# Performance work log

Measured on AMD Instinct MI355X. Metric: run time of the kernel, lower is better.

Reference implementation:

```python
import jax, jax.numpy as jnp
import numpy as np

KH, KW, STRIDE, PAD = 3, 3, 1, 1


def unfold(img, kh, kw, stride, padding):
    # torch.nn.functional.unfold, transposed to [B, L, C*kh*kw] with (c, kh, kw)-major ordering
    b, c, h, w = img.shape
    p = jnp.pad(img, ((0, 0), (0, 0), (padding, padding), (padding, padding)))
    oh = (h - kh + 2 * padding) // stride + 1
    ow = (w - kw + 2 * padding) // stride + 1
    # [b, c, kh*kw, oh, ow]; static python loop over the 9 kernel offsets only
    cols = jnp.stack([p[:, :, i:i + oh * stride:stride, j:j + ow * stride:stride]
                      for i in range(kh) for j in range(kw)], axis=2)
    return cols.reshape(b, c * kh * kw, oh * ow).transpose(0, 2, 1), oh, ow


def setup_inputs() -> dict:
    key = jax.random.key(0)
    k1, k2 = jax.random.split(key)
    img = jax.random.normal(k1, (8, 64, 112, 112), dtype=jnp.float32)
    weights = 0.8 * jax.random.normal(k2, (64, 64, 3, 3), dtype=jnp.float32)
    return {"img": img, "weights": weights}


def reference(img, weights):
    b = img.shape[0]
    O = weights.shape[0]
    W = weights.reshape(O, -1)            # [O, K], K = in_ch*kh*kw
    K = W.shape[1]
    u, oh, ow = unfold(img, KH, KW, STRIDE, PAD)   # [b, L, K]
    u2 = u * u
    u3 = u2 * u

    def gemm(poly):
        return jnp.einsum('blk,ok->blo', poly, W)

    # f: identity-kernel term has all-zero coefficients (p00=p10=p20=p30=0) -> drops out
    f = gemm(-0.000287 + 0.266 * u - 0.1097 * u2) / 75

    # identity_kernel is all ones, so (const*ones) @ ones.T == const * K (scalar)
    g1 = (0.11 / 75) * K + gemm(0.001309 + 0.00619 * u - 0.009 * u2 + 0.001383 * u3)
    g2 = (0.179 / 75) * K + gemm(-0.0025 + 0.00303 * u - 0.00484 * u2 + 0.0175 * u3)
    g3 = (0.238 / 75) * K + gemm(-0.000954 + 0.00187 * u + 0.001877 * u2 + 0.01502 * u3)
    g4 = (0.388 / 75) * K + gemm(-0.00734 + 0.001117 * u + 0.00752 * u2 + 0.009 * u3)
    g5 = (0.507 / 75) * K + gemm(-0.01017 + 0.000426 * u + 0.00837 * u2 + 0.00413 * u3)

    sig = jax.nn.sigmoid
    s1 = sig(10 * (0.15 - f))
    s2 = sig(10 * (f - 0.15)) + sig(10 * (0.23 - f)) - 1
    s3 = sig(10 * (f - 0.23)) + sig(10 * (0.32 - f)) - 1
    s4 = sig(10 * (f - 0.32)) + sig(10 * (0.39 - f)) - 1
    s5 = sig(10 * (f - 0.39))

    out = s1 * g1 + s2 * g2 + s3 * g3 + s4 * g4 + s5 * g5   # [b, L, O]
    return out.transpose(0, 2, 1).reshape(b, O, oh, ow)
```

## Files before the change

### kernel.cpp

```cpp
#include <hip/hip_runtime.h>

#define HW   112
#define PH   114
#define KK   576
#define PLANE_SH (8 * PH * PH * 64)
#define WB_OFF_SH (3 * PLANE_SH)
#define S_OFF_SH  (WB_OFF_SH + 36864)

typedef __attribute__((ext_vector_type(8))) short s16x8;
typedef __attribute__((ext_vector_type(4))) float f32x4;
typedef __attribute__((address_space(3))) unsigned int lds_u32;
typedef const __attribute__((address_space(1))) unsigned int glb_u32;

__device__ inline unsigned short f2bf(float f) {
    unsigned u = __float_as_uint(f);
    u += 0x7FFF + ((u >> 16) & 1);
    return (unsigned short)(u >> 16);
}

__global__ void border_kernel(unsigned short* __restrict__ pw) {
    const int bid = blockIdx.x;
    const int p = bid >> 3, b = bid & 7;
    unsigned short* base = pw + (size_t)p * PLANE_SH + (size_t)b * PH * PH * 64;
    const int t = threadIdx.x;
    const s16x8 z = {0, 0, 0, 0, 0, 0, 0, 0};
    for (int i = 0; i < 15; ++i) {
        const int e = t + i * 256;
        if (e >= 3616) break;
        const int n = e >> 3, c8 = e & 7;
        int x, yy;
        if (n < 114)      { yy = 0;   x = n; }
        else if (n < 228) { yy = 113; x = n - 114; }
        else { const int m2 = n - 228; yy = 1 + (m2 >> 1); x = (m2 & 1) ? 113 : 0; }
        *(s16x8*)&base[(yy * PH + x) * 64 + c8 * 8] = z;
    }
}

__global__ __launch_bounds__(256) void pow_kernel(const float* __restrict__ img,
                                                  unsigned short* __restrict__ pw) {
    __shared__ __align__(16) unsigned short sA[3 * 112 * 72];
    const int t = threadIdx.x;
    const int bid = blockIdx.x;
    const int b = bid / 112, y = bid - b * 112;

    const int c = t & 63, xq0 = t >> 6;
    const float4* src = (const float4*)(img + (((size_t)(b * 64 + c) * HW + y) * HW));
    #pragma unroll
    for (int i = 0; i < 7; ++i) {
        const int xq = xq0 + i * 4;
        const float4 v = src[xq];
        const float vv[4] = {v.x, v.y, v.z, v.w};
        #pragma unroll
        for (int u = 0; u < 4; ++u) {
            const float v1 = vv[u], v2 = v1 * v1, v3 = v2 * v1;
            const int x = xq * 4 + u;
            sA[x * 72 + c]         = f2bf(v1);
            sA[8064 + x * 72 + c]  = f2bf(v2);
            sA[16128 + x * 72 + c] = f2bf(v3);
        }
    }
    __syncthreads();

    for (int i = 0; i < 11; ++i) {
        const int ch = t + i * 256;
        if (ch >= 2688) break;
        const int p = ch / 896, r = ch - p * 896;
        const int x = r >> 3, c8 = r & 7;
        const s16x8 val = *(const s16x8*)&sA[p * 8064 + x * 72 + c8 * 8];
        *(s16x8*)&pw[(size_t)p * PLANE_SH + ((size_t)(b * PH + y + 1) * PH + (x + 1)) * 64 + c8 * 8] = val;
    }
}

__global__ void prep_kernel(const float* __restrict__ W,
                            unsigned short* __restrict__ wb,
                            float* __restrict__ S) {
    __shared__ float partial[256];
    const int bid = blockIdx.x, t = threadIdx.x;
    if (bid < 144) {
        const int i   = bid * 256 + t;
        const int j   = i & 7;
        const int l   = (i >> 3) & 63;
        const int nt  = (i >> 9) & 3;
        const int cc  = (i >> 11) & 1;
        const int tap = i >> 12;
        const int c   = cc * 32 + ((l >> 4) << 3) + j;
        const int o   = nt * 16 + (l & 15);
        wb[i] = f2bf(W[o * KK + c * 9 + tap]);
    } else {
        const int o = t >> 2, part = t & 3;
        const float4* row = (const float4*)(W + o * KK) + part * 36;
        float s = 0.f;
        for (int k = 0; k < 36; ++k) { float4 v = row[k]; s += v.x + v.y + v.z + v.w; }
        partial[t] = s;
        __syncthreads();
        if (part == 0) S[o] = partial[t] + partial[t + 1] + partial[t + 2] + partial[t + 3];
    }
}

__global__ __launch_bounds__(128, 3) void conv_main(const unsigned short* __restrict__ pw,
                                                    const unsigned short* __restrict__ wb,
                                                    const float* __restrict__ S,
                                                    float* __restrict__ out) {
    __shared__ __align__(16) unsigned short tile[1296 * 8];

    const int t = threadIdx.x, wv = t >> 6, lane = t & 63;
    const int m = lane & 15, q = lane >> 4;

    const int bid = blockIdx.x;
    const int b = bid & 7;
    const int r = bid >> 3;
    const int ty = r / 7, tx = r - ty * 7;
    const int y0 = ty * 4, x0 = tx * 16;

    f32x4 acc[3][2][4];
    #pragma unroll
    for (int p = 0; p < 3; ++p)
        #pragma unroll
        for (int at = 0; at < 2; ++at)
            #pragma unroll
            for (int nt = 0; nt < 4; ++nt)
                acc[p][at][nt] = (f32x4){0.f, 0.f, 0.f, 0.f};

    const unsigned short* pbase = pw + ((size_t)(b * PH + y0) * PH + x0) * 64;

    for (int cc = 0; cc < 2; ++cc) {
        if (cc) __syncthreads();
        const int coff = cc * 32;
        for (int i = 0; i < 10; ++i) {
            const int g = i * 128 + t;
            const int px = g / 12, rem = g - px * 12;
            const int pp = rem >> 2, qq = rem & 3;
            const int yy = px / 18, xx = px - yy * 18;
            const unsigned short* gp = pbase + (size_t)pp * PLANE_SH + (yy * PH + xx) * 64 + coff + qq * 8;
            lds_u32* lp = (lds_u32*)(unsigned short*)(tile + (size_t)(i * 128 + wv * 64) * 8);
            __builtin_amdgcn_global_load_lds((glb_u32*)gp, lp, 16, 0, 0);
        }
        if (t < 16) {
            const int g = 1280 + t;
            const int px = g / 12, rem = g - px * 12;
            const int pp = rem >> 2, qq = rem & 3;
            const int yy = px / 18, xx = px - yy * 18;
            const s16x8 v = *(const s16x8*)(pbase + (size_t)pp * PLANE_SH + (yy * PH + xx) * 64 + coff + qq * 8);
            *(s16x8*)&tile[g * 8] = v;
        }
        __syncthreads();

        #pragma unroll 3
        for (int tap = 0; tap < 9; ++tap) {
            const int ky = tap / 3, kx = tap - 3 * ky;
            s16x8 bf[4];
            const uint4* wbase = (const uint4*)wb + ((size_t)(tap * 2 + cc) * 4) * 64 + lane;
            #pragma unroll
            for (int nt = 0; nt < 4; ++nt)
                bf[nt] = *(const s16x8*)(wbase + nt * 64);
            #pragma unroll
            for (int at = 0; at < 2; ++at) {
                const int px = (2 * wv + at + ky) * 18 + m + kx;
                const int abase = px * 96 + q * 8;
                #pragma unroll
                for (int p = 0; p < 3; ++p) {
                    const s16x8 af = *(const s16x8*)&tile[abase + p * 32];
                    #pragma unroll
                    for (int nt = 0; nt < 4; ++nt)
                        acc[p][at][nt] = __builtin_amdgcn_mfma_f32_16x16x32_bf16(
                            af, bf[nt], acc[p][at][nt], 0, 0, 0);
                }
            }
        }
    }

    #pragma unroll
    for (int nt = 0; nt < 4; ++nt) {
        const int o = nt * 16 + (lane & 15);
        const float Sv = S[o];
        const float fS = -0.000287f / 75.f * Sv;
        const float b1 = 0.8448f   + 0.001309f  * Sv;
        const float b2 = 1.37472f  - 0.0025f    * Sv;
        const float b3 = 1.82784f  - 0.000954f  * Sv;
        const float b4 = 2.97984f  - 0.00734f   * Sv;
        const float b5 = 3.89376f  - 0.01017f   * Sv;
        #pragma unroll
        for (int at = 0; at < 2; ++at) {
            float res[4];
            #pragma unroll
            for (int rg = 0; rg < 4; ++rg) {
                const float u1 = acc[0][at][nt][rg];
                const float u2 = acc[1][at][nt][rg];
                const float u3 = acc[2][at][nt][rg];
                const float f  = fS + 0.00354667f * u1 - 0.00146267f * u2;
                const float g1 = b1 + 0.00619f  * u1 - 0.009f    * u2 + 0.001383f * u3;
                const float g2 = b2 + 0.00303f  * u1 - 0.00484f  * u2 + 0.0175f   * u3;
                const float g3 = b3 + 0.00187f  * u1 + 0.001877f * u2 + 0.01502f  * u3;
                const float g4 = b4 + 0.001117f * u1 + 0.00752f  * u2 + 0.009f    * u3;
                const float g5 = b5 + 0.000426f * u1 + 0.00837f  * u2 + 0.00413f  * u3;
                const float E  = __expf(-10.f * f);
                const float s1 = __builtin_amdgcn_rcpf(1.f + E * 4.4816890703f);
                const float s2 = __builtin_amdgcn_rcpf(1.f + E * 9.9741824548f);
                const float s3 = __builtin_amdgcn_rcpf(1.f + E * 24.5325301971f);
                const float s4 = __builtin_amdgcn_rcpf(1.f + E * 49.4024491055f);
                res[rg] = g1 + s1 * (g2 - g1) + s2 * (g3 - g2) + s3 * (g4 - g3) + s4 * (g5 - g4);
            }
            const int y = y0 + 2 * wv + at;
            float* op = out + (((size_t)(b * 64 + o)) * HW + y) * HW + x0 + q * 4;
            *(float4*)op = make_float4(res[0], res[1], res[2], res[3]);
        }
    }
}

extern "C" void kernel_launch(void* const* d_in, const int* in_sizes, int n_in,
                              void* d_out, int out_size, void* d_ws, size_t ws_size,
                              hipStream_t stream) {
    const float* img = (const float*)d_in[0];
    const float* w   = (const float*)d_in[1];
    float* outp = (float*)d_out;
    unsigned short* pw = (unsigned short*)d_ws;
    unsigned short* wb = pw + WB_OFF_SH;
    float* S = (float*)(pw + S_OFF_SH);

    hipLaunchKernelGGL(border_kernel, dim3(24),   dim3(256), 0, stream, pw);
    hipLaunchKernelGGL(pow_kernel,    dim3(896),  dim3(256), 0, stream, img, pw);
    hipLaunchKernelGGL(prep_kernel,   dim3(145),  dim3(256), 0, stream, w, wb, S);
    hipLaunchKernelGGL(conv_main,     dim3(1568), dim3(128), 0, stream, pw, wb, S, outp);
}
```

Before: 126.3 us.

## Drop LDS staging in conv_main and read activations directly from global memory

The conv kernel no longer stages the padded input tile through shared memory with global_load_lds and barriers. Each wave now loads its A fragments straight from global memory per kx and reuses them across the three ky taps via register rows, and the loop is restructured around kx/ky. Blocks grow to 256 threads covering 8 output rows with half as many blocks. This removes LDS traffic and synchronisation, at the cost of more redundant global and L2 reads and higher register pressure.

```diff
diff --git a/kernel.cpp b/kernel.cpp
--- a/kernel.cpp
+++ b/kernel.cpp
@@ -9,8 +9,6 @@
 
 typedef __attribute__((ext_vector_type(8))) short s16x8;
 typedef __attribute__((ext_vector_type(4))) float f32x4;
-typedef __attribute__((address_space(3))) unsigned int lds_u32;
-typedef const __attribute__((address_space(1))) unsigned int glb_u32;
 
 __device__ inline unsigned short f2bf(float f) {
     unsigned u = __float_as_uint(f);
@@ -97,20 +95,18 @@
     }
 }
 
-__global__ __launch_bounds__(128, 3) void conv_main(const unsigned short* __restrict__ pw,
+__global__ __launch_bounds__(256, 2) void conv_main(const unsigned short* __restrict__ pw,
                                                     const unsigned short* __restrict__ wb,
                                                     const float* __restrict__ S,
                                                     float* __restrict__ out) {
-    __shared__ __align__(16) unsigned short tile[1296 * 8];
-
     const int t = threadIdx.x, wv = t >> 6, lane = t & 63;
     const int m = lane & 15, q = lane >> 4;
 
     const int bid = blockIdx.x;
     const int b = bid & 7;
-    const int r = bid >> 3;
-    const int ty = r / 7, tx = r - ty * 7;
-    const int y0 = ty * 4, x0 = tx * 16;
+    const int rr = bid >> 3;
+    const int ty = rr / 7, tx = rr - ty * 7;
+    const int Y0 = ty * 8, X0 = tx * 16;
 
     f32x4 acc[3][2][4];
     #pragma unroll
@@ -121,51 +117,41 @@
             for (int nt = 0; nt < 4; ++nt)
                 acc[p][at][nt] = (f32x4){0.f, 0.f, 0.f, 0.f};
 
-    const unsigned short* pbase = pw + ((size_t)(b * PH + y0) * PH + x0) * 64;
-
+    const char* pb = (const char*)(pw + (size_t)b * PH * PH * 64);
+    int vofs[4];
+    #pragma unroll
+    for (int r4 = 0; r4 < 4; ++r4)
+        vofs[r4] = ((Y0 + 2 * wv + r4) * PH + X0 + m) * 128 + q * 16;
+
+    #pragma unroll 1
     for (int cc = 0; cc < 2; ++cc) {
-        if (cc) __syncthreads();
-        const int coff = cc * 32;
-        for (int i = 0; i < 10; ++i) {
-            const int g = i * 128 + t;
-            const int px = g / 12, rem = g - px * 12;
-            const int pp = rem >> 2, qq = rem & 3;
-            const int yy = px / 18, xx = px - yy * 18;
-            const unsigned short* gp = pbase + (size_t)pp * PLANE_SH + (yy * PH + xx) * 64 + coff + qq * 8;
-            lds_u32* lp = (lds_u32*)(unsigned short*)(tile + (size_t)(i * 128 + wv * 64) * 8);
-            __builtin_amdgcn_global_load_lds((glb_u32*)gp, lp, 16, 0, 0);
-        }
-        if (t < 16) {
-            const int g = 1280 + t;
-            const int px = g / 12, rem = g - px * 12;
-            const int pp = rem >> 2, qq = rem & 3;
-            const int yy = px / 18, xx = px - yy * 18;
-            const s16x8 v = *(const s16x8*)(pbase + (size_t)pp * PLANE_SH + (yy * PH + xx) * 64 + coff + qq * 8);
-            *(s16x8*)&tile[g * 8] = v;
-        }
-        __syncthreads();
-
-        #pragma unroll 3
-        for (int tap = 0; tap < 9; ++tap) {
-            const int ky = tap / 3, kx = tap - 3 * ky;
-            s16x8 bf[4];
-            const uint4* wbase = (const uint4*)wb + ((size_t)(tap * 2 + cc) * 4) * 64 + lane;
-            #pragma unroll
-            for (int nt = 0; nt < 4; ++nt)
-                bf[nt] = *(const s16x8*)(wbase + nt * 64);
-            #pragma unroll
-            for (int at = 0; at < 2; ++at) {
-                const int px = (2 * wv + at + ky) * 18 + m + kx;
-                const int abase = px * 96 + q * 8;
+        #pragma unroll
+        for (int kx = 0; kx < 3; ++kx) {
+            s16x8 bf[3][4];
+            #pragma unroll
+            for (int ky = 0; ky < 3; ++ky) {
+                const int tap = ky * 3 + kx;
                 #pragma unroll
-                for (int p = 0; p < 3; ++p) {
-                    const s16x8 af = *(const s16x8*)&tile[abase + p * 32];
+                for (int nt = 0; nt < 4; ++nt)
+                    bf[ky][nt] = *(const s16x8*)&wb[(((tap * 2 + cc) * 4 + nt) * 64 + lane) * 8];
+            }
+            s16x8 af[4][3];
+            #pragma unroll
+            for (int r4 = 0; r4 < 4; ++r4)
+                #pragma unroll
+                for (int p = 0; p < 3; ++p)
+                    af[r4][p] = *(const s16x8*)(pb + (size_t)p * (PLANE_SH * 2)
+                                                + vofs[r4] + kx * 128 + cc * 64);
+            #pragma unroll
+            for (int ky = 0; ky < 3; ++ky)
+                #pragma unroll
+                for (int at = 0; at < 2; ++at)
                     #pragma unroll
-                    for (int nt = 0; nt < 4; ++nt)
-                        acc[p][at][nt] = __builtin_amdgcn_mfma_f32_16x16x32_bf16(
-                            af, bf[nt], acc[p][at][nt], 0, 0, 0);
-                }
-            }
+                    for (int p = 0; p < 3; ++p)
+                        #pragma unroll
+                        for (int nt = 0; nt < 4; ++nt)
+                            acc[p][at][nt] = __builtin_amdgcn_mfma_f32_16x16x32_bf16(
+                                af[at + ky][p], bf[ky][nt], acc[p][at][nt], 0, 0, 0);
         }
     }
 
@@ -200,8 +186,8 @@
                 const float s4 = __builtin_amdgcn_rcpf(1.f + E * 49.4024491055f);
                 res[rg] = g1 + s1 * (g2 - g1) + s2 * (g3 - g2) + s3 * (g4 - g3) + s4 * (g5 - g4);
             }
-            const int y = y0 + 2 * wv + at;
-            float* op = out + (((size_t)(b * 64 + o)) * HW + y) * HW + x0 + q * 4;
+            const int y = Y0 + 2 * wv + at;
+            float* op = out + (((size_t)(b * 64 + o)) * HW + y) * HW + X0 + q * 4;
             *(float4*)op = make_float4(res[0], res[1], res[2], res[3]);
         }
     }
@@ -217,8 +203,8 @@
     unsigned short* wb = pw + WB_OFF_SH;
     float* S = (float*)(pw + S_OFF_SH);
 
-    hipLaunchKernelGGL(border_kernel, dim3(24),   dim3(256), 0, stream, pw);
-    hipLaunchKernelGGL(pow_kernel,    dim3(896),  dim3(256), 0, stream, img, pw);
-    hipLaunchKernelGGL(prep_kernel,   dim3(145),  dim3(256), 0, stream, w, wb, S);
-    hipLaunchKernelGGL(conv_main,     dim3(1568), dim3(128), 0, stream, pw, wb, S, outp);
-}
+    hipLaunchKernelGGL(border_kernel, dim3(24),  dim3(256), 0, stream, pw);
+    hipLaunchKernelGGL(pow_kernel,    dim3(896), dim3(256), 0, stream, img, pw);
+    hipLaunchKernelGGL(prep_kernel,   dim3(145), dim3(256), 0, stream, w, wb, S);
+    hipLaunchKernelGGL(conv_main,     dim3(784), dim3(256), 0, stream, pw, wb, S, outp);
+}
```

Result: slower. 141.3 us (+11.8%).
